# Kernel tuning notes

Hardware: AMD Instinct MI355X
Metric: run time of the kernel (lower is better)

## Reference

```python
import jax, jax.numpy as jnp
import numpy as np

B, HW, N, C, F, ITERS = 32, 4096, 16, 128, 512, 3
EPS_LN = 1e-5
EPS_ATTN = 1e-5


def _ln(x, g, b):
    m = x.mean(-1, keepdims=True)
    v = ((x - m) ** 2).mean(-1, keepdims=True)
    return (x - m) / jnp.sqrt(v + EPS_LN) * g + b


def _gru(x, h, wih, whh, bih, bhh):
    # torch.nn.GRUCell math
    gi = x @ wih.T + bih
    gh = h @ whh.T + bhh
    i_r, i_z, i_n = jnp.split(gi, 3, axis=-1)
    h_r, h_z, h_n = jnp.split(gh, 3, axis=-1)
    r = jax.nn.sigmoid(i_r + h_r)
    z = jax.nn.sigmoid(i_z + h_z)
    n = jnp.tanh(i_n + r * h_n)
    return (1.0 - z) * n + z * h


def setup_inputs() -> dict:
    key = jax.random.key(0)
    ks = jax.random.split(key, 16)
    s = 0.02
    d = {
        'inp': jax.random.normal(ks[0], (B, HW, C), jnp.float32),
        'query': jax.random.normal(ks[1], (B, N, C), jnp.float32),
        'ln_kv_g': jnp.ones((C,), jnp.float32),
        'ln_kv_b': jnp.zeros((C,), jnp.float32),
        'Wk': jax.random.normal(ks[2], (C, C), jnp.float32) * s,
        'Wv': jax.random.normal(ks[3], (C, C), jnp.float32) * s,
        'ln_q_g': jnp.ones((C,), jnp.float32),
        'ln_q_b': jnp.zeros((C,), jnp.float32),
        'Wq': jax.random.normal(ks[4], (C, C), jnp.float32) * s,
        'gru_wih': jax.random.normal(ks[5], (3 * C, C), jnp.float32) * s,
        'gru_whh': jax.random.normal(ks[6], (3 * C, C), jnp.float32) * s,
        'gru_bih': jnp.zeros((3 * C,), jnp.float32),
        'gru_bhh': jnp.zeros((3 * C,), jnp.float32),
        'ln2_g': jnp.ones((C,), jnp.float32),
        'ln2_b': jnp.zeros((C,), jnp.float32),
        'ffn_w1': jax.random.normal(ks[7], (F, C), jnp.float32) * s,
        'ffn_b1': jnp.zeros((F,), jnp.float32),
        'ffn_w2': jax.random.normal(ks[8], (C, F), jnp.float32) * s,
        'ffn_b2': jnp.zeros((C,), jnp.float32),
    }
    return d


def reference(inp, query, ln_kv_g, ln_kv_b, Wk, Wv, ln_q_g, ln_q_b, Wq,
              gru_wih, gru_whh, gru_bih, gru_bhh, ln2_g, ln2_b,
              ffn_w1, ffn_b1, ffn_w2, ffn_b2):
    b, n, c = query.shape
    kv = _ln(inp, ln_kv_g, ln_kv_b)
    k = kv @ Wk.T  # (b, hw, c)
    v = kv @ Wv.T  # (b, hw, c)
    scale = c ** -0.5
    q = query
    a0 = None
    for _ in range(ITERS):
        x = q
        qn = _ln(q, ln_q_g, ln_q_b) @ Wq.T
        logit = jnp.einsum('bqc,bkc->bqk', qn * scale, k)  # (b, n, hw)
        a0 = jax.nn.softmax(logit, axis=1)  # inverted: softmax over slots
        a = a0 / (a0.sum(2, keepdims=True) + EPS_ATTN)  # renorm over keys
        u = jnp.einsum('bqk,bkc->bqc', a, v)
        y = _gru(u.reshape(b * n, c), x.reshape(b * n, c),
                 gru_wih, gru_whh, gru_bih, gru_bhh).reshape(b, n, c)
        z = _ln(y, ln2_g, ln2_b)
        ffn = jax.nn.relu(z @ ffn_w1.T + ffn_b1) @ ffn_w2.T + ffn_b2
        q = y + ffn
    return (q, a0)
```

## Files before the change

### kernel.cpp

```cpp
#include <hip/hip_runtime.h>
#include <math.h>

#define B_ 32
#define HW_ 4096
#define N_ 16
#define C_ 128
#define F_ 512
#define ITERS_ 3
#define EPS_LN 1e-5f
#define EPS_ATTN 1e-5f

typedef __attribute__((ext_vector_type(8))) short short8;
typedef __attribute__((ext_vector_type(4))) float f32x4;

static __device__ __forceinline__ unsigned short f2b(float f) {
    union { float f; unsigned u; } v; v.f = f;
    unsigned r = v.u + 0x7fffu + ((v.u >> 16) & 1u);
    return (unsigned short)(r >> 16);
}
static __device__ __forceinline__ float blo(unsigned u) {
    union { unsigned u; float f; } v; v.u = u << 16; return v.f;
}
static __device__ __forceinline__ float bhi(unsigned u) {
    union { unsigned u; float f; } v; v.u = u & 0xffff0000u; return v.f;
}

__global__ __launch_bounds__(256) void k_prep(
    const float* __restrict__ Wk, const float* __restrict__ Wv,
    const float* __restrict__ wih, const float* __restrict__ whh,
    const float* __restrict__ w1, const float* __restrict__ w2,
    unsigned short* __restrict__ Wk_bf, unsigned short* __restrict__ Wv_bf,
    unsigned short* __restrict__ wih_bf, unsigned short* __restrict__ whh_bf,
    unsigned short* __restrict__ w1_bf, unsigned short* __restrict__ w2_bf,
    const float* __restrict__ query, const float* __restrict__ lnqg,
    const float* __restrict__ lnqb, const float* __restrict__ Wq,
    unsigned short* __restrict__ qn_g)
{
    __shared__ __align__(16) float xq[16 * 128];
    int tid = threadIdx.x;
    if (blockIdx.x < 256) {
        int t = blockIdx.x * 256 + tid;
        const float* src; unsigned short* dst; int off;
        if (t < 4096)       { src = Wk;  dst = Wk_bf;  off = t; }
        else if (t < 8192)  { src = Wv;  dst = Wv_bf;  off = t - 4096; }
        else if (t < 20480) { src = wih; dst = wih_bf; off = t - 8192; }
        else if (t < 32768) { src = whh; dst = whh_bf; off = t - 20480; }
        else if (t < 49152) { src = w1;  dst = w1_bf;  off = t - 32768; }
        else                { src = w2;  dst = w2_bf;  off = t - 49152; }
        float4 a = ((const float4*)src)[off];
        uint2 p;
        p.x = (unsigned)f2b(a.x) | ((unsigned)f2b(a.y) << 16);
        p.y = (unsigned)f2b(a.z) | ((unsigned)f2b(a.w) << 16);
        *(uint2*)(dst + off * 4) = p;
        return;
    }
    int b = blockIdx.x - 256;
    int n = tid >> 4, part = tid & 15;
    int row = b * 16 + n;
    const float4* x4 = (const float4*)(query + row * 128 + part * 8);
    float4 x0 = x4[0], x1 = x4[1];
    float s = x0.x + x0.y + x0.z + x0.w + x1.x + x1.y + x1.z + x1.w;
    float ss = x0.x * x0.x + x0.y * x0.y + x0.z * x0.z + x0.w * x0.w +
               x1.x * x1.x + x1.y * x1.y + x1.z * x1.z + x1.w * x1.w;
    s += __shfl_xor(s, 1); s += __shfl_xor(s, 2); s += __shfl_xor(s, 4); s += __shfl_xor(s, 8);
    ss += __shfl_xor(ss, 1); ss += __shfl_xor(ss, 2); ss += __shfl_xor(ss, 4); ss += __shfl_xor(ss, 8);
    float mean = s * (1.f / 128.f);
    float var = ss * (1.f / 128.f) - mean * mean;
    float rstd = rsqrtf(var + EPS_LN);
    const float4* g4 = (const float4*)(lnqg + part * 8);
    const float4* b4 = (const float4*)(lnqb + part * 8);
    float4 g0 = g4[0], g1 = g4[1], bb0 = b4[0], bb1 = b4[1];
    float4 o0, o1;
    o0.x = (x0.x - mean) * rstd * g0.x + bb0.x;
    o0.y = (x0.y - mean) * rstd * g0.y + bb0.y;
    o0.z = (x0.z - mean) * rstd * g0.z + bb0.z;
    o0.w = (x0.w - mean) * rstd * g0.w + bb0.w;
    o1.x = (x1.x - mean) * rstd * g1.x + bb1.x;
    o1.y = (x1.y - mean) * rstd * g1.y + bb1.y;
    o1.z = (x1.z - mean) * rstd * g1.z + bb1.z;
    o1.w = (x1.w - mean) * rstd * g1.w + bb1.w;
    float4* xrow = (float4*)&xq[n * 128];
    xrow[part * 2] = o0;
    xrow[part * 2 + 1] = o1;
    __syncthreads();
    float o[8] = {0.f, 0.f, 0.f, 0.f, 0.f, 0.f, 0.f, 0.f};
    const float4* xv4 = (const float4*)&xq[n * 128];
#pragma unroll 4
    for (int j = 0; j < 32; j++) {
        float4 xv = xv4[j];
#pragma unroll
        for (int i = 0; i < 8; i++) {
            float4 w = ((const float4*)(Wq + (part * 8 + i) * 128))[j];
            o[i] += w.x * xv.x + w.y * xv.y + w.z * xv.z + w.w * xv.w;
        }
    }
    const float scale = 0.08838834764831845f;
#pragma unroll
    for (int i = 0; i < 8; i++)
        qn_g[row * 128 + part * 8 + i] = f2b(o[i] * scale);
}

__global__ __launch_bounds__(256) void k_kvproj(
    const float* __restrict__ inp, const float* __restrict__ lng,
    const float* __restrict__ lnb, const unsigned short* __restrict__ Wk_bf,
    const unsigned short* __restrict__ Wv_bf, unsigned short* __restrict__ Kbf,
    unsigned short* __restrict__ Vt)
{
    __shared__ __align__(16) unsigned short W_lds[128 * 128];
    __shared__ __align__(16) unsigned short T_lds[8960];
    const int tid = threadIdx.x;
    const int wave = tid >> 6, lane = tid & 63;
    const int l15 = lane & 15, q4 = lane >> 4;
    const int kof = q4 * 8;
    const int tile0 = blockIdx.x * 64;
    const int b = tile0 >> 12;
    const int hwbase = tile0 & (HW_ - 1);

    const int srow = tid >> 1, shalf = tid & 1;
    const int sswz = srow & 7;

    float x[4][8];
    {
        const float* rowp = inp + (tile0 + (wave << 4) + l15) * C_;
        float s = 0.f, ss = 0.f;
#pragma unroll
        for (int ks = 0; ks < 4; ks++) {
#pragma unroll
            for (int h = 0; h < 2; h++) {
                float4 v = *(const float4*)(rowp + ks * 32 + kof + h * 4);
                x[ks][h * 4 + 0] = v.x; x[ks][h * 4 + 1] = v.y;
                x[ks][h * 4 + 2] = v.z; x[ks][h * 4 + 3] = v.w;
                s += v.x + v.y + v.z + v.w;
                ss += v.x * v.x + v.y * v.y + v.z * v.z + v.w * v.w;
            }
        }
        s += __shfl_xor(s, 16);  s += __shfl_xor(s, 32);
        ss += __shfl_xor(ss, 16); ss += __shfl_xor(ss, 32);
        float mean = s * (1.f / 128.f);
        float var = ss * (1.f / 128.f) - mean * mean;
        float rstd = rsqrtf(var + EPS_LN);
#pragma unroll
        for (int ks = 0; ks < 4; ks++) {
#pragma unroll
            for (int h = 0; h < 2; h++) {
                float4 g = *(const float4*)(lng + ks * 32 + kof + h * 4);
                float4 bb = *(const float4*)(lnb + ks * 32 + kof + h * 4);
                x[ks][h * 4 + 0] = (x[ks][h * 4 + 0] - mean) * rstd * g.x + bb.x;
                x[ks][h * 4 + 1] = (x[ks][h * 4 + 1] - mean) * rstd * g.y + bb.y;
                x[ks][h * 4 + 2] = (x[ks][h * 4 + 2] - mean) * rstd * g.z + bb.z;
                x[ks][h * 4 + 3] = (x[ks][h * 4 + 3] - mean) * rstd * g.w + bb.w;
            }
        }
    }
    short8 af[4];
#pragma unroll
    for (int ks = 0; ks < 4; ks++) {
        union { short8 s8; unsigned u[4]; } p;
#pragma unroll
        for (int j = 0; j < 4; j++)
            p.u[j] = (unsigned)f2b(x[ks][2 * j]) | ((unsigned)f2b(x[ks][2 * j + 1]) << 16);
        af[ks] = p.s8;
    }

    {
        const uint4* gW = (const uint4*)Wk_bf;
#pragma unroll
        for (int j = 0; j < 8; j++) {
            int c = shalf * 8 + j;
            uint4 w = gW[srow * 16 + c];
            *(uint4*)&W_lds[srow * 128 + (c ^ sswz) * 8] = w;
        }
    }
    __syncthreads();

    f32x4 acc[8];
#pragma unroll
    for (int nt = 0; nt < 8; nt++) {
        acc[nt] = (f32x4){0.f, 0.f, 0.f, 0.f};
#pragma unroll
        for (int ks = 0; ks < 4; ks++) {
            short8 bf = *(const short8*)&W_lds[(nt * 16 + l15) * 128 + ((ks * 4 + q4) ^ (l15 & 7)) * 8];
            acc[nt] = __builtin_amdgcn_mfma_f32_16x16x32_bf16(af[ks], bf, acc[nt], 0, 0, 0);
        }
    }
#pragma unroll
    for (int nt = 0; nt < 8; nt++) {
        int c = nt * 16 + l15;
#pragma unroll
        for (int i = 0; i < 4; i++)
            T_lds[((wave << 4) + (q4 << 2) + i) * 132 + c] = f2b(acc[nt][i]);
    }
    __syncthreads();
    {
        int row = tid >> 2, part = tid & 3;
        uint4* dst = (uint4*)&Kbf[(b * HW_ + hwbase + row) * C_ + part * 32];
#pragma unroll
        for (int j = 0; j < 4; j++)
            dst[j] = *(const uint4*)&T_lds[row * 132 + part * 32 + j * 8];
    }
    {
        const uint4* gW = (const uint4*)Wv_bf;
#pragma unroll
        for (int j = 0; j < 8; j++) {
            int c = shalf * 8 + j;
            uint4 w = gW[srow * 16 + c];
            *(uint4*)&W_lds[srow * 128 + (c ^ sswz) * 8] = w;
        }
    }
    __syncthreads();
#pragma unroll
    for (int nt = 0; nt < 8; nt++) {
        acc[nt] = (f32x4){0.f, 0.f, 0.f, 0.f};
#pragma unroll
        for (int ks = 0; ks < 4; ks++) {
            short8 bf = *(const short8*)&W_lds[(nt * 16 + l15) * 128 + ((ks * 4 + q4) ^ (l15 & 7)) * 8];
            acc[nt] = __builtin_amdgcn_mfma_f32_16x16x32_bf16(af[ks], bf, acc[nt], 0, 0, 0);
        }
    }
    __syncthreads();
#pragma unroll
    for (int nt = 0; nt < 8; nt++) {
        int c = nt * 16 + l15;
#pragma unroll
        for (int i = 0; i < 4; i++)
            T_lds[c * 70 + (wave << 4) + (q4 << 2) + i] = f2b(acc[nt][i]);
    }
    __syncthreads();
    {
        int c = tid >> 1, half = tid & 1;
        uint4* dst = (uint4*)&Vt[(b * C_ + c) * HW_ + hwbase + half * 32];
#pragma unroll
        for (int j = 0; j < 4; j++)
            dst[j] = *(const uint4*)&T_lds[c * 70 + half * 32 + j * 8];
    }
}

__global__ __launch_bounds__(128) void k_attn(
    const unsigned short* __restrict__ qn_g, const unsigned short* __restrict__ Kbf,
    const unsigned short* __restrict__ Vt, float* __restrict__ Upart,
    float* __restrict__ rspart, float* __restrict__ a0_out, int last)
{
    __shared__ __align__(16) float Ul[2][16 * 132];
    __shared__ __align__(16) unsigned short Pb[2][16 * 72];
    __shared__ float rsw[2][16];
    const int b = blockIdx.y, chunk = blockIdx.x;
    const int tid = threadIdx.x;
    const int wave = tid >> 6, lane = tid & 63;
    const int l15 = lane & 15, q4 = lane >> 4;
    const int kof = q4 * 8;
    const int hwb = chunk * 128 + wave * 64;

    short8 aq[4];
#pragma unroll
    for (int ks = 0; ks < 4; ks++)
        aq[ks] = *(const short8*)&qn_g[(b * 16 + l15) * 128 + ks * 32 + kof];
    short8 av[8][2];
#pragma unroll
    for (int ct = 0; ct < 8; ct++) {
#pragma unroll
        for (int k2 = 0; k2 < 2; k2++)
            av[ct][k2] = *(const short8*)&Vt[(b * C_ + ct * 16 + l15) * HW_ + hwb + k2 * 32 + kof];
    }

    unsigned short* Pw = &Pb[wave][0];
    float rs[4] = {0.f, 0.f, 0.f, 0.f};
#pragma unroll
    for (int s = 0; s < 4; s++) {
        int hwt = hwb + s * 16;
        f32x4 sa = {0.f, 0.f, 0.f, 0.f};
#pragma unroll
        for (int ks = 0; ks < 4; ks++) {
            short8 bk = *(const short8*)&Kbf[(b * HW_ + hwt + l15) * C_ + ks * 32 + kof];
            sa = __builtin_amdgcn_mfma_f32_16x16x32_bf16(aq[ks], bk, sa, 0, 0, 0);
        }
        float mx = fmaxf(fmaxf(sa[0], sa[1]), fmaxf(sa[2], sa[3]));
        mx = fmaxf(mx, __shfl_xor(mx, 16));
        mx = fmaxf(mx, __shfl_xor(mx, 32));
        float e[4]; float ssum = 0.f;
#pragma unroll
        for (int i = 0; i < 4; i++) { e[i] = __expf(sa[i] - mx); ssum += e[i]; }
        ssum += __shfl_xor(ssum, 16);
        ssum += __shfl_xor(ssum, 32);
        float inv = 1.f / ssum;
#pragma unroll
        for (int i = 0; i < 4; i++) {
            float a0v = e[i] * inv;
            rs[i] += a0v;
            if (last) a0_out[(b * 16 + q4 * 4 + i) * HW_ + hwt + l15] = a0v;
            Pw[(q4 * 4 + i) * 72 + s * 16 + l15] = f2b(a0v);
        }
    }
#pragma unroll
    for (int i = 0; i < 4; i++) {
        rs[i] += __shfl_xor(rs[i], 1);
        rs[i] += __shfl_xor(rs[i], 2);
        rs[i] += __shfl_xor(rs[i], 4);
        rs[i] += __shfl_xor(rs[i], 8);
    }
    if (l15 == 0) {
#pragma unroll
        for (int i = 0; i < 4; i++) rsw[wave][q4 * 4 + i] = rs[i];
    }
    short8 bp0 = *(const short8*)&Pw[l15 * 72 + kof];
    short8 bp1 = *(const short8*)&Pw[l15 * 72 + 32 + kof];
#pragma unroll
    for (int ct = 0; ct < 8; ct++) {
        f32x4 ua = __builtin_amdgcn_mfma_f32_16x16x32_bf16(av[ct][0], bp0, (f32x4){0.f, 0.f, 0.f, 0.f}, 0, 0, 0);
        ua = __builtin_amdgcn_mfma_f32_16x16x32_bf16(av[ct][1], bp1, ua, 0, 0, 0);
        *(f32x4*)&Ul[wave][l15 * 132 + ct * 16 + (q4 << 2)] = ua;
    }
    __syncthreads();
    {
        float* up = Upart + (b * 32 + chunk) * 2048;
#pragma unroll
        for (int k = 0; k < 16; k++) {
            int idx = tid + k * 128;
            int q = idx >> 7, c = idx & 127;
            up[idx] = Ul[0][q * 132 + c] + Ul[1][q * 132 + c];
        }
        if (tid < 16)
            rspart[(b * 32 + chunk) * 16 + tid] = rsw[0][tid] + rsw[1][tid];
    }
}

__global__ __launch_bounds__(256) void k_tail(
    const float* __restrict__ Upart, const float* __restrict__ rspart,
    const float* __restrict__ hsrc, float* __restrict__ q_buf,
    const unsigned short* __restrict__ wih_bf, const unsigned short* __restrict__ whh_bf,
    const float* __restrict__ bih, const float* __restrict__ bhh,
    const float* __restrict__ ln2g, const float* __restrict__ ln2b,
    const unsigned short* __restrict__ w1_bf, const float* __restrict__ b1,
    const unsigned short* __restrict__ w2_bf, const float* __restrict__ b2,
    const float* __restrict__ lnqg, const float* __restrict__ lnqb,
    const float* __restrict__ Wq, unsigned short* __restrict__ qn_g,
    float* __restrict__ out_q, int last)
{
    __shared__ __align__(16) float u_l[128];
    __shared__ __align__(16) float h_l[128];
    __shared__ __align__(16) float g_l[768];
    __shared__ __align__(16) float z_l[128];
    __shared__ __align__(16) float y_l[128];
    __shared__ __align__(16) float h1_l[512];
    __shared__ __align__(16) float red[256];
    __shared__ float stats[2];
    __shared__ float srs;
    const int tid = threadIdx.x;
    const int row = blockIdx.x;
    const int b = row >> 4, q = row & 15;
    const int lane = tid & 63;

    {
        int c = tid & 127, h = tid >> 7;
        float part = 0.f;
#pragma unroll
        for (int ch = 0; ch < 16; ch++)
            part += Upart[(b * 32 + h * 16 + ch) * 2048 + q * 128 + c];
        red[tid] = part;
        if (tid < 128) h_l[tid] = hsrc[row * 128 + tid];
        if (tid < 64) {
            float v = (lane < 32) ? rspart[(b * 32 + lane) * 16 + q] : 0.f;
#pragma unroll
            for (int off = 1; off < 64; off <<= 1) v += __shfl_xor(v, off);
            if (tid == 0) srs = v;
        }
    }
    __syncthreads();
    if (tid < 128)
        u_l[tid] = (red[tid] + red[tid + 128]) / (srs + EPS_ATTN);
    __syncthreads();
#pragma unroll
    for (int o3 = 0; o3 < 3; o3++) {
        int o = tid + o3 * 256;
        const unsigned short* wrow;
        const float* src;
        float bias;
        if (o < 384) { wrow = wih_bf + o * 128; src = u_l; bias = bih[o]; }
        else         { wrow = whh_bf + (o - 384) * 128; src = h_l; bias = bhh[o - 384]; }
        const uint4* w4 = (const uint4*)wrow;
        const float4* s4 = (const float4*)src;
        float acc = 0.f;
#pragma unroll 8
        for (int j = 0; j < 16; j++) {
            uint4 w = w4[j];
            float4 aA = s4[2 * j], aB = s4[2 * j + 1];
            acc += blo(w.x) * aA.x + bhi(w.x) * aA.y + blo(w.y) * aA.z + bhi(w.y) * aA.w
                 + blo(w.z) * aB.x + bhi(w.z) * aB.y + blo(w.w) * aB.z + bhi(w.w) * aB.w;
        }
        g_l[o] = acc + bias;
    }
    __syncthreads();
    if (tid < 128) {
        int c = tid;
        float ir = g_l[c], iz = g_l[128 + c], in_ = g_l[256 + c];
        float hr = g_l[384 + c], hz = g_l[512 + c], hn = g_l[640 + c];
        float rr = 1.f / (1.f + expf(-(ir + hr)));
        float zz = 1.f / (1.f + expf(-(iz + hz)));
        float nn = tanhf(in_ + rr * hn);
        y_l[c] = (1.f - zz) * nn + zz * h_l[c];
    }
    __syncthreads();
    if (tid < 64) {
        float v0 = y_l[lane], v1 = y_l[lane + 64];
        float s = v0 + v1, ss = v0 * v0 + v1 * v1;
#pragma unroll
        for (int off = 1; off < 64; off <<= 1) {
            s += __shfl_xor(s, off);
            ss += __shfl_xor(ss, off);
        }
        if (tid == 0) {
            float mean = s * (1.f / 128.f);
            float var = ss * (1.f / 128.f) - mean * mean;
            stats[0] = mean;
            stats[1] = rsqrtf(var + EPS_LN);
        }
    }
    __syncthreads();
    if (tid < 128)
        z_l[tid] = (y_l[tid] - stats[0]) * stats[1] * ln2g[tid] + ln2b[tid];
    __syncthreads();
#pragma unroll
    for (int f2i = 0; f2i < 2; f2i++) {
        int f = tid + f2i * 256;
        const uint4* w4 = (const uint4*)(w1_bf + f * 128);
        const float4* s4 = (const float4*)z_l;
        float acc = 0.f;
#pragma unroll 8
        for (int j = 0; j < 16; j++) {
            uint4 w = w4[j];
            float4 aA = s4[2 * j], aB = s4[2 * j + 1];
            acc += blo(w.x) * aA.x + bhi(w.x) * aA.y + blo(w.y) * aA.z + bhi(w.y) * aA.w
                 + blo(w.z) * aB.x + bhi(w.z) * aB.y + blo(w.w) * aB.z + bhi(w.w) * aB.w;
        }
        h1_l[f] = fmaxf(acc + b1[f], 0.f);
    }
    __syncthreads();
    {
        int c = tid & 127, h = tid >> 7;
        const uint4* w4 = (const uint4*)(w2_bf + c * 512 + h * 256);
        const float4* hh = (const float4*)&h1_l[h * 256];
        float acc = 0.f;
#pragma unroll 8
        for (int j = 0; j < 32; j++) {
            uint4 w = w4[j];
            float4 hA = hh[2 * j], hB = hh[2 * j + 1];
            acc += blo(w.x) * hA.x + bhi(w.x) * hA.y + blo(w.y) * hA.z + bhi(w.y) * hA.w
                 + blo(w.z) * hB.x + bhi(w.z) * hB.y + blo(w.w) * hB.z + bhi(w.w) * hB.w;
        }
        red[tid] = acc;
    }
    __syncthreads();
    float q_new = 0.f;
    if (tid < 128) {
        q_new = y_l[tid] + red[tid] + red[tid + 128] + b2[tid];
        q_buf[row * 128 + tid] = q_new;
        if (last) out_q[row * 128 + tid] = q_new;
    }
    if (!last) {
        __syncthreads();
        if (tid < 128) y_l[tid] = q_new;
        __syncthreads();
        if (tid < 64) {
            float v0 = y_l[lane], v1 = y_l[lane + 64];
            float s = v0 + v1, ss = v0 * v0 + v1 * v1;
#pragma unroll
            for (int off = 1; off < 64; off <<= 1) {
                s += __shfl_xor(s, off);
                ss += __shfl_xor(ss, off);
            }
            if (tid == 0) {
                float mean = s * (1.f / 128.f);
                float var = ss * (1.f / 128.f) - mean * mean;
                stats[0] = mean;
                stats[1] = rsqrtf(var + EPS_LN);
            }
        }
        __syncthreads();
        if (tid < 128)
            z_l[tid] = (y_l[tid] - stats[0]) * stats[1] * lnqg[tid] + lnqb[tid];
        __syncthreads();
        {
            int c = tid & 127, h = tid >> 7;
            const float4* w4 = (const float4*)(Wq + c * 128 + h * 64);
            const float4* zz = (const float4*)&z_l[h * 64];
            float acc = 0.f;
#pragma unroll 8
            for (int j = 0; j < 16; j++) {
                float4 w = w4[j], v = zz[j];
                acc += w.x * v.x + w.y * v.y + w.z * v.z + w.w * v.w;
            }
            red[tid] = acc;
        }
        __syncthreads();
        if (tid < 128)
            qn_g[row * 128 + tid] = f2b((red[tid] + red[tid + 128]) * 0.08838834764831845f);
    }
}

extern "C" void kernel_launch(void* const* d_in, const int* in_sizes, int n_in,
                              void* d_out, int out_size, void* d_ws, size_t ws_size,
                              hipStream_t stream) {
    const float* inp     = (const float*)d_in[0];
    const float* query   = (const float*)d_in[1];
    const float* ln_kv_g = (const float*)d_in[2];
    const float* ln_kv_b = (const float*)d_in[3];
    const float* Wk      = (const float*)d_in[4];
    const float* Wv      = (const float*)d_in[5];
    const float* ln_q_g  = (const float*)d_in[6];
    const float* ln_q_b  = (const float*)d_in[7];
    const float* Wq      = (const float*)d_in[8];
    const float* gru_wih = (const float*)d_in[9];
    const float* gru_whh = (const float*)d_in[10];
    const float* gru_bih = (const float*)d_in[11];
    const float* gru_bhh = (const float*)d_in[12];
    const float* ln2_g   = (const float*)d_in[13];
    const float* ln2_b   = (const float*)d_in[14];
    const float* ffn_w1  = (const float*)d_in[15];
    const float* ffn_b1  = (const float*)d_in[16];
    const float* ffn_w2  = (const float*)d_in[17];
    const float* ffn_b2  = (const float*)d_in[18];

    char* ws = (char*)d_ws;
    unsigned short* Kbf    = (unsigned short*)ws;
    unsigned short* Vt     = (unsigned short*)(ws + 33554432);
    float* q_buf           = (float*)(ws + 67108864);
    float* Upart           = (float*)(ws + 67371008);
    float* rspart          = (float*)(ws + 75759616);
    unsigned short* qn_g   = (unsigned short*)(ws + 75825152);
    unsigned short* Wk_bf  = (unsigned short*)(ws + 75956224);
    unsigned short* Wv_bf  = (unsigned short*)(ws + 75988992);
    unsigned short* wih_bf = (unsigned short*)(ws + 76021760);
    unsigned short* whh_bf = (unsigned short*)(ws + 76120064);
    unsigned short* w1_bf  = (unsigned short*)(ws + 76218368);
    unsigned short* w2_bf  = (unsigned short*)(ws + 76349440);

    float* out_q  = (float*)d_out;
    float* out_a0 = out_q + B_ * N_ * C_;

    k_prep<<<dim3(288), dim3(256), 0, stream>>>(
        Wk, Wv, gru_wih, gru_whh, ffn_w1, ffn_w2,
        Wk_bf, Wv_bf, wih_bf, whh_bf, w1_bf, w2_bf,
        query, ln_q_g, ln_q_b, Wq, qn_g);
    k_kvproj<<<dim3((B_ * HW_) / 64), dim3(256), 0, stream>>>(
        inp, ln_kv_g, ln_kv_b, Wk_bf, Wv_bf, Kbf, Vt);

    for (int it = 0; it < ITERS_; it++) {
        int last = (it == ITERS_ - 1) ? 1 : 0;
        const float* hsrc = (it == 0) ? query : q_buf;
        k_attn<<<dim3(32, B_), dim3(128), 0, stream>>>(
            qn_g, Kbf, Vt, Upart, rspart, out_a0, last);
        k_tail<<<dim3(B_ * N_), dim3(256), 0, stream>>>(
            Upart, rspart, hsrc, q_buf, wih_bf, whh_bf, gru_bih, gru_bhh,
            ln2_g, ln2_b, w1_bf, ffn_b1, w2_bf, ffn_b2,
            ln_q_g, ln_q_b, Wq, qn_g, out_q, last);
    }
}
```

Measured before the change: 332.4 us.

## Load Wk and Wv together and store K/V directly from MFMA outputs

Result: no change. 334.4 us (+0.6%).

```diff
diff --git a/kernel.cpp b/kernel.cpp
--- a/kernel.cpp
+++ b/kernel.cpp
@@ -106,8 +106,7 @@
     const unsigned short* __restrict__ Wv_bf, unsigned short* __restrict__ Kbf,
     unsigned short* __restrict__ Vt)
 {
-    __shared__ __align__(16) unsigned short W_lds[128 * 128];
-    __shared__ __align__(16) unsigned short T_lds[8960];
+    __shared__ __align__(16) unsigned short W_lds[2][16384];
     const int tid = threadIdx.x;
     const int wave = tid >> 6, lane = tid & 63;
     const int l15 = lane & 15, q4 = lane >> 4;
@@ -116,8 +115,18 @@
     const int b = tile0 >> 12;
     const int hwbase = tile0 & (HW_ - 1);
 
-    const int srow = tid >> 1, shalf = tid & 1;
-    const int sswz = srow & 7;
+    {
+        int srow = tid >> 1, shalf = tid & 1, sswz = srow & 7;
+        const uint4* gWk = (const uint4*)Wk_bf;
+        const uint4* gWv = (const uint4*)Wv_bf;
+#pragma unroll
+        for (int j = 0; j < 8; j++) {
+            int c = shalf * 8 + j;
+            int dsto = srow * 128 + (c ^ sswz) * 8;
+            *(uint4*)&W_lds[0][dsto] = gWk[srow * 16 + c];
+            *(uint4*)&W_lds[1][dsto] = gWv[srow * 16 + c];
+        }
+    }
 
     float x[4][8];
     {
@@ -161,77 +170,27 @@
             p.u[j] = (unsigned)f2b(x[ks][2 * j]) | ((unsigned)f2b(x[ks][2 * j + 1]) << 16);
         af[ks] = p.s8;
     }
-
-    {
-        const uint4* gW = (const uint4*)Wk_bf;
-#pragma unroll
-        for (int j = 0; j < 8; j++) {
-            int c = shalf * 8 + j;
-            uint4 w = gW[srow * 16 + c];
-            *(uint4*)&W_lds[srow * 128 + (c ^ sswz) * 8] = w;
-        }
-    }
-    __syncthreads();
-
-    f32x4 acc[8];
-#pragma unroll
-    for (int nt = 0; nt < 8; nt++) {
-        acc[nt] = (f32x4){0.f, 0.f, 0.f, 0.f};
+    __syncthreads();
+
+    unsigned short* krow = &Kbf[(b * HW_ + hwbase + (wave << 4) + l15) * C_];
+    unsigned short* vbase = &Vt[b * C_ * HW_ + hwbase + (wave << 4) + (q4 << 2)];
+#pragma unroll
+    for (int ct = 0; ct < 8; ct++) {
+        f32x4 aK = {0.f, 0.f, 0.f, 0.f};
+        f32x4 aV = {0.f, 0.f, 0.f, 0.f};
 #pragma unroll
         for (int ks = 0; ks < 4; ks++) {
-            short8 bf = *(const short8*)&W_lds[(nt * 16 + l15) * 128 + ((ks * 4 + q4) ^ (l15 & 7)) * 8];
-            acc[nt] = __builtin_amdgcn_mfma_f32_16x16x32_bf16(af[ks], bf, acc[nt], 0, 0, 0);
-        }
-    }
-#pragma unroll
-    for (int nt = 0; nt < 8; nt++) {
-        int c = nt * 16 + l15;
-#pragma unroll
-        for (int i = 0; i < 4; i++)
-            T_lds[((wave << 4) + (q4 << 2) + i) * 132 + c] = f2b(acc[nt][i]);
-    }
-    __syncthreads();
-    {
-        int row = tid >> 2, part = tid & 3;
-        uint4* dst = (uint4*)&Kbf[(b * HW_ + hwbase + row) * C_ + part * 32];
-#pragma unroll
-        for (int j = 0; j < 4; j++)
-            dst[j] = *(const uint4*)&T_lds[row * 132 + part * 32 + j * 8];
-    }
-    {
-        const uint4* gW = (const uint4*)Wv_bf;
-#pragma unroll
-        for (int j = 0; j < 8; j++) {
-            int c = shalf * 8 + j;
-            uint4 w = gW[srow * 16 + c];
-            *(uint4*)&W_lds[srow * 128 + (c ^ sswz) * 8] = w;
-        }
-    }
-    __syncthreads();
-#pragma unroll
-    for (int nt = 0; nt < 8; nt++) {
-        acc[nt] = (f32x4){0.f, 0.f, 0.f, 0.f};
-#pragma unroll
-        for (int ks = 0; ks < 4; ks++) {
-            short8 bf = *(const short8*)&W_lds[(nt * 16 + l15) * 128 + ((ks * 4 + q4) ^ (l15 & 7)) * 8];
-            acc[nt] = __builtin_amdgcn_mfma_f32_16x16x32_bf16(af[ks], bf, acc[nt], 0, 0, 0);
-        }
-    }
-    __syncthreads();
-#pragma unroll
-    for (int nt = 0; nt < 8; nt++) {
-        int c = nt * 16 + l15;
-#pragma unroll
-        for (int i = 0; i < 4; i++)
-            T_lds[c * 70 + (wave << 4) + (q4 << 2) + i] = f2b(acc[nt][i]);
-    }
-    __syncthreads();
-    {
-        int c = tid >> 1, half = tid & 1;
-        uint4* dst = (uint4*)&Vt[(b * C_ + c) * HW_ + hwbase + half * 32];
-#pragma unroll
-        for (int j = 0; j < 4; j++)
-            dst[j] = *(const uint4*)&T_lds[c * 70 + half * 32 + j * 8];
+            int off = (ct * 16 + l15) * 128 + ((ks * 4 + q4) ^ (l15 & 7)) * 8;
+            short8 wk = *(const short8*)&W_lds[0][off];
+            short8 wv = *(const short8*)&W_lds[1][off];
+            aK = __builtin_amdgcn_mfma_f32_16x16x32_bf16(wk, af[ks], aK, 0, 0, 0);
+            aV = __builtin_amdgcn_mfma_f32_16x16x32_bf16(af[ks], wv, aV, 0, 0, 0);
+        }
+        union { uint2 u2; unsigned short sh[4]; } pk, pv;
+#pragma unroll
+        for (int i = 0; i < 4; i++) { pk.sh[i] = f2b(aK[i]); pv.sh[i] = f2b(aV[i]); }
+        *(uint2*)&krow[ct * 16 + (q4 << 2)] = pk.u2;
+        *(uint2*)&vbase[(ct * 16 + l15) * HW_] = pv.u2;
     }
 }
 
```

## Fuse attention and GRU/FFN tail into one kernel with per-batch atomic handoff

Applied to the files above, without the earlier changes.

Result: slower. 704.9 us (+112.1%).

```diff
diff --git a/kernel.cpp b/kernel.cpp
--- a/kernel.cpp
+++ b/kernel.cpp
@@ -34,10 +34,14 @@
     unsigned short* __restrict__ w1_bf, unsigned short* __restrict__ w2_bf,
     const float* __restrict__ query, const float* __restrict__ lnqg,
     const float* __restrict__ lnqb, const float* __restrict__ Wq,
-    unsigned short* __restrict__ qn_g)
+    unsigned short* __restrict__ qn_g, int* __restrict__ cnt)
 {
     __shared__ __align__(16) float xq[16 * 128];
     int tid = threadIdx.x;
+    if (blockIdx.x == 288) {
+        if (tid < 3 * B_) cnt[tid] = 0;
+        return;
+    }
     if (blockIdx.x < 256) {
         int t = blockIdx.x * 256 + tid;
         const float* src; unsigned short* dst; int off;
@@ -235,96 +239,10 @@
     }
 }
 
-__global__ __launch_bounds__(128) void k_attn(
-    const unsigned short* __restrict__ qn_g, const unsigned short* __restrict__ Kbf,
+__global__ __launch_bounds__(128, 3) void k_attn_tail(
+    const unsigned short* __restrict__ qn_g_ro, const unsigned short* __restrict__ Kbf,
     const unsigned short* __restrict__ Vt, float* __restrict__ Upart,
-    float* __restrict__ rspart, float* __restrict__ a0_out, int last)
-{
-    __shared__ __align__(16) float Ul[2][16 * 132];
-    __shared__ __align__(16) unsigned short Pb[2][16 * 72];
-    __shared__ float rsw[2][16];
-    const int b = blockIdx.y, chunk = blockIdx.x;
-    const int tid = threadIdx.x;
-    const int wave = tid >> 6, lane = tid & 63;
-    const int l15 = lane & 15, q4 = lane >> 4;
-    const int kof = q4 * 8;
-    const int hwb = chunk * 128 + wave * 64;
-
-    short8 aq[4];
-#pragma unroll
-    for (int ks = 0; ks < 4; ks++)
-        aq[ks] = *(const short8*)&qn_g[(b * 16 + l15) * 128 + ks * 32 + kof];
-    short8 av[8][2];
-#pragma unroll
-    for (int ct = 0; ct < 8; ct++) {
-#pragma unroll
-        for (int k2 = 0; k2 < 2; k2++)
-            av[ct][k2] = *(const short8*)&Vt[(b * C_ + ct * 16 + l15) * HW_ + hwb + k2 * 32 + kof];
-    }
-
-    unsigned short* Pw = &Pb[wave][0];
-    float rs[4] = {0.f, 0.f, 0.f, 0.f};
-#pragma unroll
-    for (int s = 0; s < 4; s++) {
-        int hwt = hwb + s * 16;
-        f32x4 sa = {0.f, 0.f, 0.f, 0.f};
-#pragma unroll
-        for (int ks = 0; ks < 4; ks++) {
-            short8 bk = *(const short8*)&Kbf[(b * HW_ + hwt + l15) * C_ + ks * 32 + kof];
-            sa = __builtin_amdgcn_mfma_f32_16x16x32_bf16(aq[ks], bk, sa, 0, 0, 0);
-        }
-        float mx = fmaxf(fmaxf(sa[0], sa[1]), fmaxf(sa[2], sa[3]));
-        mx = fmaxf(mx, __shfl_xor(mx, 16));
-        mx = fmaxf(mx, __shfl_xor(mx, 32));
-        float e[4]; float ssum = 0.f;
-#pragma unroll
-        for (int i = 0; i < 4; i++) { e[i] = __expf(sa[i] - mx); ssum += e[i]; }
-        ssum += __shfl_xor(ssum, 16);
-        ssum += __shfl_xor(ssum, 32);
-        float inv = 1.f / ssum;
-#pragma unroll
-        for (int i = 0; i < 4; i++) {
-            float a0v = e[i] * inv;
-            rs[i] += a0v;
-            if (last) a0_out[(b * 16 + q4 * 4 + i) * HW_ + hwt + l15] = a0v;
-            Pw[(q4 * 4 + i) * 72 + s * 16 + l15] = f2b(a0v);
-        }
-    }
-#pragma unroll
-    for (int i = 0; i < 4; i++) {
-        rs[i] += __shfl_xor(rs[i], 1);
-        rs[i] += __shfl_xor(rs[i], 2);
-        rs[i] += __shfl_xor(rs[i], 4);
-        rs[i] += __shfl_xor(rs[i], 8);
-    }
-    if (l15 == 0) {
-#pragma unroll
-        for (int i = 0; i < 4; i++) rsw[wave][q4 * 4 + i] = rs[i];
-    }
-    short8 bp0 = *(const short8*)&Pw[l15 * 72 + kof];
-    short8 bp1 = *(const short8*)&Pw[l15 * 72 + 32 + kof];
-#pragma unroll
-    for (int ct = 0; ct < 8; ct++) {
-        f32x4 ua = __builtin_amdgcn_mfma_f32_16x16x32_bf16(av[ct][0], bp0, (f32x4){0.f, 0.f, 0.f, 0.f}, 0, 0, 0);
-        ua = __builtin_amdgcn_mfma_f32_16x16x32_bf16(av[ct][1], bp1, ua, 0, 0, 0);
-        *(f32x4*)&Ul[wave][l15 * 132 + ct * 16 + (q4 << 2)] = ua;
-    }
-    __syncthreads();
-    {
-        float* up = Upart + (b * 32 + chunk) * 2048;
-#pragma unroll
-        for (int k = 0; k < 16; k++) {
-            int idx = tid + k * 128;
-            int q = idx >> 7, c = idx & 127;
-            up[idx] = Ul[0][q * 132 + c] + Ul[1][q * 132 + c];
-        }
-        if (tid < 16)
-            rspart[(b * 32 + chunk) * 16 + tid] = rsw[0][tid] + rsw[1][tid];
-    }
-}
-
-__global__ __launch_bounds__(256) void k_tail(
-    const float* __restrict__ Upart, const float* __restrict__ rspart,
+    float* __restrict__ rspart, float* __restrict__ a0_out,
     const float* __restrict__ hsrc, float* __restrict__ q_buf,
     const unsigned short* __restrict__ wih_bf, const unsigned short* __restrict__ whh_bf,
     const float* __restrict__ bih, const float* __restrict__ bhh,
@@ -332,168 +250,292 @@
     const unsigned short* __restrict__ w1_bf, const float* __restrict__ b1,
     const unsigned short* __restrict__ w2_bf, const float* __restrict__ b2,
     const float* __restrict__ lnqg, const float* __restrict__ lnqb,
-    const float* __restrict__ Wq, unsigned short* __restrict__ qn_g,
-    float* __restrict__ out_q, int last)
+    const float* __restrict__ Wq, unsigned short* __restrict__ qn_g_w,
+    float* __restrict__ out_q, int* __restrict__ cnt, int last)
 {
-    __shared__ __align__(16) float u_l[128];
-    __shared__ __align__(16) float h_l[128];
-    __shared__ __align__(16) float g_l[768];
-    __shared__ __align__(16) float z_l[128];
-    __shared__ __align__(16) float y_l[128];
-    __shared__ __align__(16) float h1_l[512];
-    __shared__ __align__(16) float red[256];
-    __shared__ float stats[2];
-    __shared__ float srs;
+    __shared__ __align__(16) char smem[21760];
+    const int b = blockIdx.y, chunk = blockIdx.x;
     const int tid = threadIdx.x;
-    const int row = blockIdx.x;
-    const int b = row >> 4, q = row & 15;
-    const int lane = tid & 63;
-
-    {
-        int c = tid & 127, h = tid >> 7;
-        float part = 0.f;
-#pragma unroll
-        for (int ch = 0; ch < 16; ch++)
-            part += Upart[(b * 32 + h * 16 + ch) * 2048 + q * 128 + c];
-        red[tid] = part;
-        if (tid < 128) h_l[tid] = hsrc[row * 128 + tid];
-        if (tid < 64) {
-            float v = (lane < 32) ? rspart[(b * 32 + lane) * 16 + q] : 0.f;
+
+    if (chunk >= 32) {
+        float (*u_l)[128]  = (float (*)[128])smem;
+        float (*h_l)[128]  = (float (*)[128])(smem + 1024);
+        float (*g_l)[768]  = (float (*)[768])(smem + 2048);
+        float (*z_l)[128]  = (float (*)[128])(smem + 8192);
+        float (*y_l)[128]  = (float (*)[128])(smem + 9216);
+        float (*h1_l)[512] = (float (*)[512])(smem + 10240);
+        float* stats = (float*)(smem + 14336);
+        float* srs2  = (float*)(smem + 14352);
+        const int q0 = (chunk - 32) * 2;
+        const int wv = tid >> 6, ln = tid & 63;
+
+        if (tid == 0) {
+            while (__hip_atomic_load(cnt + b, __ATOMIC_ACQUIRE, __HIP_MEMORY_SCOPE_AGENT) < 32)
+                __builtin_amdgcn_s_sleep(2);
+        }
+        __syncthreads();
+        __threadfence();
+
+        float us[2];
+#pragma unroll
+        for (int r = 0; r < 2; r++) {
+            float s = 0.f;
+#pragma unroll 8
+            for (int ch = 0; ch < 32; ch++)
+                s += Upart[(b * 32 + ch) * 2048 + (q0 + r) * 128 + tid];
+            us[r] = s;
+        }
+        {
+            float v = (ln < 32) ? rspart[(b * 32 + ln) * 16 + q0 + wv] : 0.f;
 #pragma unroll
             for (int off = 1; off < 64; off <<= 1) v += __shfl_xor(v, off);
-            if (tid == 0) srs = v;
-        }
-    }
-    __syncthreads();
-    if (tid < 128)
-        u_l[tid] = (red[tid] + red[tid + 128]) / (srs + EPS_ATTN);
-    __syncthreads();
-#pragma unroll
-    for (int o3 = 0; o3 < 3; o3++) {
-        int o = tid + o3 * 256;
-        const unsigned short* wrow;
-        const float* src;
-        float bias;
-        if (o < 384) { wrow = wih_bf + o * 128; src = u_l; bias = bih[o]; }
-        else         { wrow = whh_bf + (o - 384) * 128; src = h_l; bias = bhh[o - 384]; }
-        const uint4* w4 = (const uint4*)wrow;
-        const float4* s4 = (const float4*)src;
-        float acc = 0.f;
+            if (ln == 0) srs2[wv] = v;
+        }
+        __syncthreads();
+#pragma unroll
+        for (int r = 0; r < 2; r++) {
+            u_l[r][tid] = us[r] / (srs2[r] + EPS_ATTN);
+            h_l[r][tid] = hsrc[(b * 16 + q0 + r) * 128 + tid];
+        }
+        __syncthreads();
+#pragma unroll
+        for (int oo = 0; oo < 6; oo++) {
+            int o = tid + oo * 128;
+            const unsigned short* wrow;
+            const float* s0; const float* s1; float bias;
+            if (o < 384) { wrow = wih_bf + o * 128; s0 = u_l[0]; s1 = u_l[1]; bias = bih[o]; }
+            else         { wrow = whh_bf + (o - 384) * 128; s0 = h_l[0]; s1 = h_l[1]; bias = bhh[o - 384]; }
+            const uint4* w4 = (const uint4*)wrow;
+            const float4* a4 = (const float4*)s0;
+            const float4* b4 = (const float4*)s1;
+            float acc0 = 0.f, acc1 = 0.f;
 #pragma unroll 8
-        for (int j = 0; j < 16; j++) {
-            uint4 w = w4[j];
-            float4 aA = s4[2 * j], aB = s4[2 * j + 1];
-            acc += blo(w.x) * aA.x + bhi(w.x) * aA.y + blo(w.y) * aA.z + bhi(w.y) * aA.w
-                 + blo(w.z) * aB.x + bhi(w.z) * aB.y + blo(w.w) * aB.z + bhi(w.w) * aB.w;
-        }
-        g_l[o] = acc + bias;
-    }
-    __syncthreads();
-    if (tid < 128) {
-        int c = tid;
-        float ir = g_l[c], iz = g_l[128 + c], in_ = g_l[256 + c];
-        float hr = g_l[384 + c], hz = g_l[512 + c], hn = g_l[640 + c];
-        float rr = 1.f / (1.f + expf(-(ir + hr)));
-        float zz = 1.f / (1.f + expf(-(iz + hz)));
-        float nn = tanhf(in_ + rr * hn);
-        y_l[c] = (1.f - zz) * nn + zz * h_l[c];
-    }
-    __syncthreads();
-    if (tid < 64) {
-        float v0 = y_l[lane], v1 = y_l[lane + 64];
-        float s = v0 + v1, ss = v0 * v0 + v1 * v1;
-#pragma unroll
-        for (int off = 1; off < 64; off <<= 1) {
-            s += __shfl_xor(s, off);
-            ss += __shfl_xor(ss, off);
-        }
-        if (tid == 0) {
-            float mean = s * (1.f / 128.f);
-            float var = ss * (1.f / 128.f) - mean * mean;
-            stats[0] = mean;
-            stats[1] = rsqrtf(var + EPS_LN);
-        }
-    }
-    __syncthreads();
-    if (tid < 128)
-        z_l[tid] = (y_l[tid] - stats[0]) * stats[1] * ln2g[tid] + ln2b[tid];
-    __syncthreads();
-#pragma unroll
-    for (int f2i = 0; f2i < 2; f2i++) {
-        int f = tid + f2i * 256;
-        const uint4* w4 = (const uint4*)(w1_bf + f * 128);
-        const float4* s4 = (const float4*)z_l;
-        float acc = 0.f;
-#pragma unroll 8
-        for (int j = 0; j < 16; j++) {
-            uint4 w = w4[j];
-            float4 aA = s4[2 * j], aB = s4[2 * j + 1];
-            acc += blo(w.x) * aA.x + bhi(w.x) * aA.y + blo(w.y) * aA.z + bhi(w.y) * aA.w
-                 + blo(w.z) * aB.x + bhi(w.z) * aB.y + blo(w.w) * aB.z + bhi(w.w) * aB.w;
-        }
-        h1_l[f] = fmaxf(acc + b1[f], 0.f);
-    }
-    __syncthreads();
-    {
-        int c = tid & 127, h = tid >> 7;
-        const uint4* w4 = (const uint4*)(w2_bf + c * 512 + h * 256);
-        const float4* hh = (const float4*)&h1_l[h * 256];
-        float acc = 0.f;
-#pragma unroll 8
-        for (int j = 0; j < 32; j++) {
-            uint4 w = w4[j];
-            float4 hA = hh[2 * j], hB = hh[2 * j + 1];
-            acc += blo(w.x) * hA.x + bhi(w.x) * hA.y + blo(w.y) * hA.z + bhi(w.y) * hA.w
-                 + blo(w.z) * hB.x + bhi(w.z) * hB.y + blo(w.w) * hB.z + bhi(w.w) * hB.w;
-        }
-        red[tid] = acc;
-    }
-    __syncthreads();
-    float q_new = 0.f;
-    if (tid < 128) {
-        q_new = y_l[tid] + red[tid] + red[tid + 128] + b2[tid];
-        q_buf[row * 128 + tid] = q_new;
-        if (last) out_q[row * 128 + tid] = q_new;
-    }
-    if (!last) {
-        __syncthreads();
-        if (tid < 128) y_l[tid] = q_new;
-        __syncthreads();
-        if (tid < 64) {
-            float v0 = y_l[lane], v1 = y_l[lane + 64];
+            for (int j = 0; j < 16; j++) {
+                uint4 w = w4[j];
+                float w0 = blo(w.x), w1v = bhi(w.x), w2v = blo(w.y), w3 = bhi(w.y);
+                float w4v = blo(w.z), w5 = bhi(w.z), w6 = blo(w.w), w7 = bhi(w.w);
+                float4 aA = a4[2 * j], aB = a4[2 * j + 1];
+                float4 bA = b4[2 * j], bB = b4[2 * j + 1];
+                acc0 += w0 * aA.x + w1v * aA.y + w2v * aA.z + w3 * aA.w
+                      + w4v * aB.x + w5 * aB.y + w6 * aB.z + w7 * aB.w;
+                acc1 += w0 * bA.x + w1v * bA.y + w2v * bA.z + w3 * bA.w
+                      + w4v * bB.x + w5 * bB.y + w6 * bB.z + w7 * bB.w;
+            }
+            g_l[0][o] = acc0 + bias;
+            g_l[1][o] = acc1 + bias;
+        }
+        __syncthreads();
+#pragma unroll
+        for (int r = 0; r < 2; r++) {
+            int c = tid;
+            float ir = g_l[r][c], iz = g_l[r][128 + c], in_ = g_l[r][256 + c];
+            float hr = g_l[r][384 + c], hz = g_l[r][512 + c], hn = g_l[r][640 + c];
+            float rr = 1.f / (1.f + expf(-(ir + hr)));
+            float zz = 1.f / (1.f + expf(-(iz + hz)));
+            float nn = tanhf(in_ + rr * hn);
+            y_l[r][c] = (1.f - zz) * nn + zz * h_l[r][c];
+        }
+        __syncthreads();
+        {
+            float v0 = y_l[wv][ln], v1 = y_l[wv][ln + 64];
             float s = v0 + v1, ss = v0 * v0 + v1 * v1;
 #pragma unroll
             for (int off = 1; off < 64; off <<= 1) {
                 s += __shfl_xor(s, off);
                 ss += __shfl_xor(ss, off);
             }
-            if (tid == 0) {
+            if (ln == 0) {
                 float mean = s * (1.f / 128.f);
                 float var = ss * (1.f / 128.f) - mean * mean;
-                stats[0] = mean;
-                stats[1] = rsqrtf(var + EPS_LN);
-            }
-        }
-        __syncthreads();
-        if (tid < 128)
-            z_l[tid] = (y_l[tid] - stats[0]) * stats[1] * lnqg[tid] + lnqb[tid];
-        __syncthreads();
-        {
-            int c = tid & 127, h = tid >> 7;
-            const float4* w4 = (const float4*)(Wq + c * 128 + h * 64);
-            const float4* zz = (const float4*)&z_l[h * 64];
-            float acc = 0.f;
+                stats[wv * 2] = mean;
+                stats[wv * 2 + 1] = rsqrtf(var + EPS_LN);
+            }
+        }
+        __syncthreads();
+#pragma unroll
+        for (int r = 0; r < 2; r++)
+            z_l[r][tid] = (y_l[r][tid] - stats[r * 2]) * stats[r * 2 + 1] * ln2g[tid] + ln2b[tid];
+        __syncthreads();
+#pragma unroll
+        for (int ff = 0; ff < 4; ff++) {
+            int f = tid + ff * 128;
+            const uint4* w4 = (const uint4*)(w1_bf + f * 128);
+            const float4* a4 = (const float4*)z_l[0];
+            const float4* b4 = (const float4*)z_l[1];
+            float acc0 = 0.f, acc1 = 0.f;
 #pragma unroll 8
             for (int j = 0; j < 16; j++) {
-                float4 w = w4[j], v = zz[j];
-                acc += w.x * v.x + w.y * v.y + w.z * v.z + w.w * v.w;
-            }
-            red[tid] = acc;
-        }
-        __syncthreads();
-        if (tid < 128)
-            qn_g[row * 128 + tid] = f2b((red[tid] + red[tid + 128]) * 0.08838834764831845f);
-    }
+                uint4 w = w4[j];
+                float w0 = blo(w.x), w1v = bhi(w.x), w2v = blo(w.y), w3 = bhi(w.y);
+                float w4v = blo(w.z), w5 = bhi(w.z), w6 = blo(w.w), w7 = bhi(w.w);
+                float4 aA = a4[2 * j], aB = a4[2 * j + 1];
+                float4 bA = b4[2 * j], bB = b4[2 * j + 1];
+                acc0 += w0 * aA.x + w1v * aA.y + w2v * aA.z + w3 * aA.w
+                      + w4v * aB.x + w5 * aB.y + w6 * aB.z + w7 * aB.w;
+                acc1 += w0 * bA.x + w1v * bA.y + w2v * bA.z + w3 * bA.w
+                      + w4v * bB.x + w5 * bB.y + w6 * bB.z + w7 * bB.w;
+            }
+            float bv = b1[f];
+            h1_l[0][f] = fmaxf(acc0 + bv, 0.f);
+            h1_l[1][f] = fmaxf(acc1 + bv, 0.f);
+        }
+        __syncthreads();
+        float q_new[2];
+        {
+            const uint4* w4 = (const uint4*)(w2_bf + tid * 512);
+            const float4* hA4 = (const float4*)h1_l[0];
+            const float4* hB4 = (const float4*)h1_l[1];
+            float acc0 = 0.f, acc1 = 0.f;
+#pragma unroll 8
+            for (int j = 0; j < 64; j++) {
+                uint4 w = w4[j];
+                float w0 = blo(w.x), w1v = bhi(w.x), w2v = blo(w.y), w3 = bhi(w.y);
+                float w4v = blo(w.z), w5 = bhi(w.z), w6 = blo(w.w), w7 = bhi(w.w);
+                float4 aA = hA4[2 * j], aB = hA4[2 * j + 1];
+                float4 bA = hB4[2 * j], bB = hB4[2 * j + 1];
+                acc0 += w0 * aA.x + w1v * aA.y + w2v * aA.z + w3 * aA.w
+                      + w4v * aB.x + w5 * aB.y + w6 * aB.z + w7 * aB.w;
+                acc1 += w0 * bA.x + w1v * bA.y + w2v * bA.z + w3 * bA.w
+                      + w4v * bB.x + w5 * bB.y + w6 * bB.z + w7 * bB.w;
+            }
+            float bv = b2[tid];
+            q_new[0] = y_l[0][tid] + acc0 + bv;
+            q_new[1] = y_l[1][tid] + acc1 + bv;
+#pragma unroll
+            for (int r = 0; r < 2; r++) {
+                int row = b * 16 + q0 + r;
+                q_buf[row * 128 + tid] = q_new[r];
+                if (last) out_q[row * 128 + tid] = q_new[r];
+            }
+        }
+        if (!last) {
+            __syncthreads();
+#pragma unroll
+            for (int r = 0; r < 2; r++) y_l[r][tid] = q_new[r];
+            __syncthreads();
+            {
+                float v0 = y_l[wv][ln], v1 = y_l[wv][ln + 64];
+                float s = v0 + v1, ss = v0 * v0 + v1 * v1;
+#pragma unroll
+                for (int off = 1; off < 64; off <<= 1) {
+                    s += __shfl_xor(s, off);
+                    ss += __shfl_xor(ss, off);
+                }
+                if (ln == 0) {
+                    float mean = s * (1.f / 128.f);
+                    float var = ss * (1.f / 128.f) - mean * mean;
+                    stats[wv * 2] = mean;
+                    stats[wv * 2 + 1] = rsqrtf(var + EPS_LN);
+                }
+            }
+            __syncthreads();
+#pragma unroll
+            for (int r = 0; r < 2; r++)
+                z_l[r][tid] = (q_new[r] - stats[r * 2]) * stats[r * 2 + 1] * lnqg[tid] + lnqb[tid];
+            __syncthreads();
+            {
+                const float4* w4 = (const float4*)(Wq + tid * 128);
+                const float4* zA = (const float4*)z_l[0];
+                const float4* zB = (const float4*)z_l[1];
+                float acc0 = 0.f, acc1 = 0.f;
+#pragma unroll 8
+                for (int j = 0; j < 32; j++) {
+                    float4 w = w4[j], a = zA[j], bb = zB[j];
+                    acc0 += w.x * a.x + w.y * a.y + w.z * a.z + w.w * a.w;
+                    acc1 += w.x * bb.x + w.y * bb.y + w.z * bb.z + w.w * bb.w;
+                }
+#pragma unroll
+                for (int r = 0; r < 2; r++)
+                    qn_g_w[(b * 16 + q0 + r) * 128 + tid] =
+                        f2b((r == 0 ? acc0 : acc1) * 0.08838834764831845f);
+            }
+        }
+        return;
+    }
+
+    float (*Ul)[16 * 132] = (float (*)[16 * 132])smem;
+    unsigned short (*Pb)[16 * 72] = (unsigned short (*)[16 * 72])(smem + 16896);
+    float (*rsw)[16] = (float (*)[16])(smem + 21504);
+    const int wave = tid >> 6, lane = tid & 63;
+    const int l15 = lane & 15, q4 = lane >> 4;
+    const int kof = q4 * 8;
+    const int hwb = chunk * 128 + wave * 64;
+
+    short8 aq[4];
+#pragma unroll
+    for (int ks = 0; ks < 4; ks++)
+        aq[ks] = *(const short8*)&qn_g_ro[(b * 16 + l15) * 128 + ks * 32 + kof];
+    short8 av[8][2];
+#pragma unroll
+    for (int ct = 0; ct < 8; ct++) {
+#pragma unroll
+        for (int k2 = 0; k2 < 2; k2++)
+            av[ct][k2] = *(const short8*)&Vt[(b * C_ + ct * 16 + l15) * HW_ + hwb + k2 * 32 + kof];
+    }
+
+    unsigned short* Pw = &Pb[wave][0];
+    float rs[4] = {0.f, 0.f, 0.f, 0.f};
+#pragma unroll
+    for (int s = 0; s < 4; s++) {
+        int hwt = hwb + s * 16;
+        f32x4 sa = {0.f, 0.f, 0.f, 0.f};
+#pragma unroll
+        for (int ks = 0; ks < 4; ks++) {
+            short8 bk = *(const short8*)&Kbf[(b * HW_ + hwt + l15) * C_ + ks * 32 + kof];
+            sa = __builtin_amdgcn_mfma_f32_16x16x32_bf16(aq[ks], bk, sa, 0, 0, 0);
+        }
+        float mx = fmaxf(fmaxf(sa[0], sa[1]), fmaxf(sa[2], sa[3]));
+        mx = fmaxf(mx, __shfl_xor(mx, 16));
+        mx = fmaxf(mx, __shfl_xor(mx, 32));
+        float e[4]; float ssum = 0.f;
+#pragma unroll
+        for (int i = 0; i < 4; i++) { e[i] = __expf(sa[i] - mx); ssum += e[i]; }
+        ssum += __shfl_xor(ssum, 16);
+        ssum += __shfl_xor(ssum, 32);
+        float inv = 1.f / ssum;
+#pragma unroll
+        for (int i = 0; i < 4; i++) {
+            float a0v = e[i] * inv;
+            rs[i] += a0v;
+            if (last) a0_out[(b * 16 + q4 * 4 + i) * HW_ + hwt + l15] = a0v;
+            Pw[(q4 * 4 + i) * 72 + s * 16 + l15] = f2b(a0v);
+        }
+    }
+#pragma unroll
+    for (int i = 0; i < 4; i++) {
+        rs[i] += __shfl_xor(rs[i], 1);
+        rs[i] += __shfl_xor(rs[i], 2);
+        rs[i] += __shfl_xor(rs[i], 4);
+        rs[i] += __shfl_xor(rs[i], 8);
+    }
+    if (l15 == 0) {
+#pragma unroll
+        for (int i = 0; i < 4; i++) rsw[wave][q4 * 4 + i] = rs[i];
+    }
+    short8 bp0 = *(const short8*)&Pw[l15 * 72 + kof];
+    short8 bp1 = *(const short8*)&Pw[l15 * 72 + 32 + kof];
+#pragma unroll
+    for (int ct = 0; ct < 8; ct++) {
+        f32x4 ua = __builtin_amdgcn_mfma_f32_16x16x32_bf16(av[ct][0], bp0, (f32x4){0.f, 0.f, 0.f, 0.f}, 0, 0, 0);
+        ua = __builtin_amdgcn_mfma_f32_16x16x32_bf16(av[ct][1], bp1, ua, 0, 0, 0);
+        *(f32x4*)&Ul[wave][l15 * 132 + ct * 16 + (q4 << 2)] = ua;
+    }
+    __syncthreads();
+    {
+        float* up = Upart + (b * 32 + chunk) * 2048;
+#pragma unroll
+        for (int k = 0; k < 16; k++) {
+            int idx = tid + k * 128;
+            int q = idx >> 7, c = idx & 127;
+            up[idx] = Ul[0][q * 132 + c] + Ul[1][q * 132 + c];
+        }
+        if (tid < 16)
+            rspart[(b * 32 + chunk) * 16 + tid] = rsw[0][tid] + rsw[1][tid];
+    }
+    __threadfence();
+    __syncthreads();
+    if (tid == 0)
+        __hip_atomic_fetch_add(cnt + b, 1, __ATOMIC_RELEASE, __HIP_MEMORY_SCOPE_AGENT);
 }
 
 extern "C" void kernel_launch(void* const* d_in, const int* in_sizes, int n_in,
@@ -532,25 +574,25 @@
     unsigned short* whh_bf = (unsigned short*)(ws + 76120064);
     unsigned short* w1_bf  = (unsigned short*)(ws + 76218368);
     unsigned short* w2_bf  = (unsigned short*)(ws + 76349440);
+    int* cnt               = (int*)(ws + 76480512);
 
     float* out_q  = (float*)d_out;
     float* out_a0 = out_q + B_ * N_ * C_;
 
-    k_prep<<<dim3(288), dim3(256), 0, stream>>>(
+    k_prep<<<dim3(289), dim3(256), 0, stream>>>(
         Wk, Wv, gru_wih, gru_whh, ffn_w1, ffn_w2,
         Wk_bf, Wv_bf, wih_bf, whh_bf, w1_bf, w2_bf,
-        query, ln_q_g, ln_q_b, Wq, qn_g);
+        query, ln_q_g, ln_q_b, Wq, qn_g, cnt);
     k_kvproj<<<dim3((B_ * HW_) / 64), dim3(256), 0, stream>>>(
         inp, ln_kv_g, ln_kv_b, Wk_bf, Wv_bf, Kbf, Vt);
 
     for (int it = 0; it < ITERS_; it++) {
         int last = (it == ITERS_ - 1) ? 1 : 0;
         const float* hsrc = (it == 0) ? query : q_buf;
-        k_attn<<<dim3(32, B_), dim3(128), 0, stream>>>(
-            qn_g, Kbf, Vt, Upart, rspart, out_a0, last);
-        k_tail<<<dim3(B_ * N_), dim3(256), 0, stream>>>(
-            Upart, rspart, hsrc, q_buf, wih_bf, whh_bf, gru_bih, gru_bhh,
+        k_attn_tail<<<dim3(40, B_), dim3(128), 0, stream>>>(
+            qn_g, Kbf, Vt, Upart, rspart, out_a0,
+            hsrc, q_buf, wih_bf, whh_bf, gru_bih, gru_bhh,
             ln2_g, ln2_b, w1_bf, ffn_b1, w2_bf, ffn_b2,
-            ln_q_g, ln_q_b, Wq, qn_g, out_q, last);
-    }
-}
+            ln_q_g, ln_q_b, Wq, qn_g, out_q, cnt + it * B_, last);
+    }
+}
```
